# Performance work log

Measured on AMD Instinct MI355X. Metric: run time of the kernel, lower is better.

## Reference

```python
import jax, jax.numpy as jnp
import numpy as np

B, S, D = 2, 2048, 2048
H, KVH = 16, 4
HD = D // H  # 128


def _rope_angles(seq, head_dim):
    theta = 1.0 / (10000.0 ** (jnp.arange(0, head_dim, 2, dtype=jnp.float32) / head_dim))
    ang = jnp.arange(seq, dtype=jnp.float32)[:, None] * theta[None, :]  # [S, HD/2]
    return jnp.cos(ang), jnp.sin(ang)


def _apply_rotary(t, cos, sin):
    # t: [B, S, h, HD]; pairs are (even, odd) along last dim (view_as_complex semantics)
    tr = t[..., 0::2]
    ti = t[..., 1::2]
    c = cos[None, :, None, :]
    s = sin[None, :, None, :]
    out_r = tr * c - ti * s
    out_i = tr * s + ti * c
    return jnp.stack([out_r, out_i], axis=-1).reshape(t.shape)


def setup_inputs() -> dict:
    key = jax.random.key(0)
    ks = jax.random.split(key, 8)
    sd = 1.0 / np.sqrt(D)
    return {
        'x': jax.random.normal(ks[0], (B, S, D), dtype=jnp.float32),
        'wq': jax.random.normal(ks[1], (D, D), dtype=jnp.float32) * sd,
        'bq': jax.random.normal(ks[2], (D,), dtype=jnp.float32) * 0.01,
        'wk': jax.random.normal(ks[3], (D, KVH * HD), dtype=jnp.float32) * sd,
        'bk': jax.random.normal(ks[4], (KVH * HD,), dtype=jnp.float32) * 0.01,
        'wv': jax.random.normal(ks[5], (D, KVH * HD), dtype=jnp.float32) * sd,
        'bv': jax.random.normal(ks[6], (KVH * HD,), dtype=jnp.float32) * 0.01,
        'wo': jax.random.normal(ks[7], (D, D), dtype=jnp.float32) * sd,
    }


def reference(x, wq, bq, wk, bk, wv, bv, wo):
    b, s, d = x.shape
    q = (x @ wq + bq).reshape(b, s, H, HD)
    k = (x @ wk + bk).reshape(b, s, KVH, HD)
    v = (x @ wv + bv).reshape(b, s, KVH, HD)

    cos, sin = _rope_angles(s, HD)
    q = _apply_rotary(q, cos, sin)
    k = _apply_rotary(k, cos, sin)

    repeat = H // KVH
    k = jnp.repeat(k, repeat, axis=2)  # [B, S, H, HD]
    v = jnp.repeat(v, repeat, axis=2)

    scale = 1.0 / np.sqrt(HD)
    att_score = jnp.einsum('bqhd,bkhd->bqhk', q, k) * scale  # [B, S, H, S]
    att_weight = jax.nn.softmax(att_score, axis=-1)
    out = jnp.einsum('bqhk,bkhd->bqhd', att_weight, v)
    out = out.reshape(b, s, H * HD)
    return out @ wo
```

## Files before the change

kernel.cpp:

```cpp
#include <hip/hip_runtime.h>
#include <hip/hip_bf16.h>
#include <cstdint>

typedef __attribute__((ext_vector_type(4))) float f32x4;
typedef __attribute__((ext_vector_type(16))) float f32x16;
typedef __attribute__((ext_vector_type(8))) short bf16x8;
typedef __attribute__((ext_vector_type(4))) unsigned int u32x4;
typedef unsigned short u16;
typedef unsigned int u32;

__device__ __forceinline__ u16 f2b(float x) {
  __hip_bfloat16 h = __float2bfloat16(x);
  return *reinterpret_cast<u16*>(&h);
}

__device__ __forceinline__ u32 pk(float a, float b) {
  return ((u32)f2b(b) << 16) | (u32)f2b(a);
}

__device__ __forceinline__ void gload16(const void* g, void* l) {
  __builtin_amdgcn_global_load_lds((const __attribute__((address_space(1))) u32*)g,
                                   (__attribute__((address_space(3))) u32*)l, 16, 0, 0);
}


__global__ void cvt_f32_bf16(const float* __restrict__ in, u16* __restrict__ out, int n4) {
  int idx = (blockIdx.x * 256 + threadIdx.x);
  if (idx < n4) {
    const float4 v = *(const float4*)(in + (size_t)idx * 4);
    u16* o = out + (size_t)idx * 4;
    o[0] = f2b(v.x); o[1] = f2b(v.y); o[2] = f2b(v.z); o[3] = f2b(v.w);
  }
}

__global__ void w_transpose_cvt(const float* __restrict__ w0, const float* __restrict__ w1,
                                const float* __restrict__ w2, int b0, int b1,
                                int N0, int N1, int N2,
                                u16* __restrict__ out, int K) {
  __shared__ float tile[32][33];
  int k0 = blockIdx.x * 32, n0 = blockIdx.y * 32;
  const float* src; int srcN; int c0;
  if (n0 < b0)      { src = w0; srcN = N0; c0 = n0; }
  else if (n0 < b1) { src = w1; srcN = N1; c0 = n0 - b0; }
  else              { src = w2; srcN = N2; c0 = n0 - b1; }
  int tx = threadIdx.x & 31, ty = threadIdx.x >> 5;
#pragma unroll
  for (int j = 0; j < 32; j += 8)
    tile[ty + j][tx] = src[(size_t)(k0 + ty + j) * srcN + c0 + tx];
  __syncthreads();
#pragma unroll
  for (int j = 0; j < 32; j += 8)
    out[(size_t)(n0 + ty + j) * K + k0 + tx] = f2b(tile[tx][ty + j]);
}

__global__ void pack_bias(const float* __restrict__ bq, const float* __restrict__ bk,
                          const float* __restrict__ bv, float* __restrict__ out) {
  int i = blockIdx.x * 256 + threadIdx.x;
  if (i < 3072) out[i] = (i < 2048) ? bq[i] : ((i < 2560) ? bk[i - 2048] : bv[i - 2560]);
}

__global__ void v_transpose_cvt(const float* __restrict__ qkv, u16* __restrict__ vt) {
  __shared__ float tile[32][33];
  int s0 = blockIdx.x * 32;
  int d0 = blockIdx.y * 32;
  int z = blockIdx.z;
  int b = z >> 2, kvh = z & 3;
  int tx = threadIdx.x & 31, ty = threadIdx.x >> 5;
#pragma unroll
  for (int j = 0; j < 32; j += 8)
    tile[ty + j][tx] = qkv[((size_t)(b * 2048 + s0 + ty + j)) * 3072 + 2560 + kvh * 128 + d0 + tx];
  __syncthreads();
#pragma unroll
  for (int j = 0; j < 32; j += 8)
    vt[((size_t)z * 128 + d0 + ty + j) * 2048 + s0 + tx] = f2b(tile[tx][ty + j]);
}

__global__ void rope_cvt(const float* __restrict__ qkv, u16* __restrict__ out,
                         int lognh, int col0, float scale) {
  int idx = blockIdx.x * 256 + threadIdx.x;
  int i = idx & 63;
  int nh = 1 << lognh;
  int h = (idx >> 6) & (nh - 1);
  int bs = idx >> (6 + lognh);
  int s = bs & 2047;
  int b = bs >> 11;
  const float* src = qkv + (size_t)bs * 3072 + col0 + h * 128 + 2 * i;
  float tr = src[0], ti = src[1];
  float theta = expf(-(float)i * 0.14391156831212787f);
  float ang = (float)s * theta;
  float sv, cv;
  sincosf(ang, &sv, &cv);
  float orr = (tr * cv - ti * sv) * scale;
  float oii = (tr * sv + ti * cv) * scale;
  u16* dst = out + (((size_t)(b * nh + h) * 2048 + s) * 128 + 2 * i);
  dst[0] = f2b(orr);
  dst[1] = f2b(oii);
}

__global__ __launch_bounds__(256) void gemm_bt_bf16(
    const u16* __restrict__ A, const u16* __restrict__ Bt,
    const float* __restrict__ bias, float* __restrict__ C,
    int M, int N, int K) {
  __shared__ u16 As[128 * 32];
  __shared__ u16 Bs[128 * 32];
  const int tid = threadIdx.x;
  const int lane = tid & 63;
  const int w = tid >> 6;
  const int wr = w >> 1, wc = w & 1;
  const int m0 = blockIdx.y * 128;
  const int n0 = blockIdx.x * 128;

  f32x4 acc[4][4] = {};

  for (int k0 = 0; k0 < K; k0 += 32) {
#pragma unroll
    for (int it = 0; it < 2; ++it) {
      int c = tid + it * 256;
      int row = c >> 2;
      int off = (c & 3) * 8;
      gload16(A + (size_t)(m0 + row) * K + k0 + off, (u16*)As + w * 512 + it * 2048);
      gload16(Bt + (size_t)(n0 + row) * K + k0 + off, (u16*)Bs + w * 512 + it * 2048);
    }
    __syncthreads();
    const int col8 = (lane >> 4) * 8;
    bf16x8 a[4], bfr[4];
#pragma unroll
    for (int m = 0; m < 4; ++m)
      a[m] = *(const bf16x8*)&As[(wr * 64 + m * 16 + (lane & 15)) * 32 + col8];
#pragma unroll
    for (int n = 0; n < 4; ++n)
      bfr[n] = *(const bf16x8*)&Bs[(wc * 64 + n * 16 + (lane & 15)) * 32 + col8];
#pragma unroll
    for (int m = 0; m < 4; ++m)
#pragma unroll
      for (int n = 0; n < 4; ++n)
        acc[m][n] = __builtin_amdgcn_mfma_f32_16x16x32_bf16(a[m], bfr[n], acc[m][n], 0, 0, 0);
    __syncthreads();
  }

#pragma unroll
  for (int m = 0; m < 4; ++m) {
    int row = m0 + wr * 64 + m * 16 + ((lane >> 4) << 2);
#pragma unroll
    for (int n = 0; n < 4; ++n) {
      int col = n0 + wc * 64 + n * 16 + (lane & 15);
      float bvv = bias ? bias[col] : 0.f;
      float* cp = C + (size_t)row * N + col;
#pragma unroll
      for (int r = 0; r < 4; ++r) cp[(size_t)r * N] = acc[m][n][r] + bvv;
    }
  }
}

__global__ __launch_bounds__(256) void flash_attn(
    const u16* __restrict__ Qr, const u16* __restrict__ Kr,
    const u16* __restrict__ Vt, u16* __restrict__ Att) {
  __shared__ u16 Ks[2][64 * 128];
  __shared__ u16 Vs[2][128 * 64];
  const int tid = threadIdx.x, lane = tid & 63, w = tid >> 6;
  const int lo = lane & 31, hi = lane >> 5;
  const int q0 = blockIdx.x * 128 + w * 32;
  const int h = blockIdx.y, b = blockIdx.z;
  const int kvh = h >> 2;

  const char* Khead = (const char*)(Kr + (size_t)(b * 4 + kvh) * 2048 * 128);
  const char* Vhead = (const char*)(Vt + (size_t)(b * 4 + kvh) * 128 * 2048);

  bf16x8 qf[8];
  {
    const u16* qp = Qr + ((size_t)(b * 16 + h) * 2048 + q0 + lo) * 128 + hi * 8;
#pragma unroll
    for (int ds = 0; ds < 8; ++ds) qf[ds] = *(const bf16x8*)(qp + ds * 16);
  }

  int koff[4], voff[4];
#pragma unroll
  for (int it = 0; it < 4; ++it) {
    int c = tid + it * 256;
    int krow = c >> 4;
    koff[it] = krow * 256 + (((c & 15) * 16) ^ ((krow & 7) << 4));
    int vrow = c >> 3;
    voff[it] = vrow * 4096 + (((c & 7) * 16) ^ ((vrow & 7) << 4));
  }

#define STAGE(bufi, t)                                                \
  {                                                                   \
    _Pragma("unroll")                                                 \
    for (int it = 0; it < 4; ++it) {                                  \
      gload16(Khead + (size_t)(t) * 16384 + koff[it],                 \
              (u16*)Ks[bufi] + it * 2048 + w * 512);                  \
      gload16(Vhead + (size_t)(t) * 128 + voff[it],                   \
              (u16*)Vs[bufi] + it * 2048 + w * 512);                  \
    }                                                                 \
  }

  f32x16 o0 = {}, o1 = {}, o2 = {}, o3 = {};
  float m_run = -3.0e38f, l_run = 0.f;
  const int swz = (lane & 7) << 4;
  const int hi16 = hi * 16;

  STAGE(0, 0);
  __syncthreads();

  int buf = 0;
  for (int t = 0; t < 32; ++t) {
    if (t < 31) { STAGE(buf ^ 1, t + 1); }

    const char* Kb = (const char*)Ks[buf];
    const char* Vb = (const char*)Vs[buf];

    f32x16 sc0 = {}, sc1 = {};
    __builtin_amdgcn_s_setprio(1);
#pragma unroll
    for (int ds = 0; ds < 8; ++ds) {
      bf16x8 kf = *(const bf16x8*)(Kb + lo * 256 + ((ds * 32 + hi16) ^ swz));
      sc0 = __builtin_amdgcn_mfma_f32_32x32x16_bf16(kf, qf[ds], sc0, 0, 0, 0);
    }
#pragma unroll
    for (int ds = 0; ds < 8; ++ds) {
      bf16x8 kf = *(const bf16x8*)(Kb + (32 + lo) * 256 + ((ds * 32 + hi16) ^ swz));
      sc1 = __builtin_amdgcn_mfma_f32_32x32x16_bf16(kf, qf[ds], sc1, 0, 0, 0);
    }
    __builtin_amdgcn_s_setprio(0);

    float pmax = sc0[0];
#pragma unroll
    for (int r = 1; r < 16; ++r) pmax = fmaxf(pmax, sc0[r]);
#pragma unroll
    for (int r = 0; r < 16; ++r) pmax = fmaxf(pmax, sc1[r]);
    pmax = fmaxf(pmax, __shfl_xor(pmax, 32, 64));

    if (!__all(pmax - m_run <= 8.0f)) {
      float mnew = fmaxf(m_run, pmax);
      float rs = __expf(m_run - mnew);
      m_run = mnew;
      l_run *= rs;
#pragma unroll
      for (int r = 0; r < 16; ++r) {
        float rsr = __shfl(rs, (r & 3) + 8 * (r >> 2) + 4 * hi, 64);
        o0[r] *= rsr; o1[r] *= rsr; o2[r] *= rsr; o3[r] *= rsr;
      }
    }

    float lsum = 0.f;
#pragma unroll
    for (int r = 0; r < 16; ++r) { float p = __expf(sc0[r] - m_run); sc0[r] = p; lsum += p; }
#pragma unroll
    for (int r = 0; r < 16; ++r) { float p = __expf(sc1[r] - m_run); sc1[r] = p; lsum += p; }
    lsum += __shfl_xor(lsum, 32, 64);
    l_run += lsum;

#define MKPA(P, s, dst)                                               \
    {                                                                 \
      u32 a0 = pk(P[8*(s)+0], P[8*(s)+1]);                            \
      u32 a1 = pk(P[8*(s)+2], P[8*(s)+3]);                            \
      u32 b0 = pk(P[8*(s)+4], P[8*(s)+5]);                            \
      u32 b1 = pk(P[8*(s)+6], P[8*(s)+7]);                            \
      u32 t0 = hi ? a0 : b0, t1 = hi ? a1 : b1;                       \
      u32 r0 = __shfl_xor(t0, 32, 64), r1 = __shfl_xor(t1, 32, 64);   \
      u32x4 wv;                                                       \
      wv[0] = hi ? r0 : a0; wv[1] = hi ? r1 : a1;                     \
      wv[2] = hi ? b0 : r0; wv[3] = hi ? b1 : r1;                     \
      dst = __builtin_bit_cast(bf16x8, wv);                           \
    }
    bf16x8 pa0, pa1, pa2, pa3;
    MKPA(sc0, 0, pa0)
    MKPA(sc0, 1, pa1)
    MKPA(sc1, 0, pa2)
    MKPA(sc1, 1, pa3)

    __builtin_amdgcn_s_setprio(1);
#define PVN(on, n)                                                                                    \
    {                                                                                                 \
      const char* vrb = Vb + ((n) * 32 + lo) * 128;                                                   \
      on = __builtin_amdgcn_mfma_f32_32x32x16_bf16(pa0, *(const bf16x8*)(vrb + ((0   + hi16) ^ swz)), on, 0, 0, 0); \
      on = __builtin_amdgcn_mfma_f32_32x32x16_bf16(pa1, *(const bf16x8*)(vrb + ((32  + hi16) ^ swz)), on, 0, 0, 0); \
      on = __builtin_amdgcn_mfma_f32_32x32x16_bf16(pa2, *(const bf16x8*)(vrb + ((64  + hi16) ^ swz)), on, 0, 0, 0); \
      on = __builtin_amdgcn_mfma_f32_32x32x16_bf16(pa3, *(const bf16x8*)(vrb + ((96  + hi16) ^ swz)), on, 0, 0, 0); \
    }
    PVN(o0, 0)
    PVN(o1, 1)
    PVN(o2, 2)
    PVN(o3, 3)
    __builtin_amdgcn_s_setprio(0);

    __syncthreads();
    buf ^= 1;
  }

  float inv = 1.0f / l_run;
  size_t rowbase = (size_t)(b * 2048 + q0);
#pragma unroll
  for (int r = 0; r < 16; ++r) {
    int rr = (r & 3) + 8 * (r >> 2) + 4 * hi;
    float invr = __shfl(inv, rr, 64);
    u16* op = Att + (rowbase + rr) * 2048 + h * 128 + lo;
    op[0]  = f2b(o0[r] * invr);
    op[32] = f2b(o1[r] * invr);
    op[64] = f2b(o2[r] * invr);
    op[96] = f2b(o3[r] * invr);
  }
}


extern "C" void kernel_launch(void* const* d_in, const int* in_sizes, int n_in,
                              void* d_out, int out_size, void* d_ws, size_t ws_size,
                              hipStream_t stream) {
  const float* x  = (const float*)d_in[0];
  const float* wq = (const float*)d_in[1];
  const float* bq = (const float*)d_in[2];
  const float* wk = (const float*)d_in[3];
  const float* bk = (const float*)d_in[4];
  const float* wv = (const float*)d_in[5];
  const float* bv = (const float*)d_in[6];
  const float* wo = (const float*)d_in[7];
  float* out = (float*)d_out;
  char* ws = (char*)d_ws;

  u16*   x_bf   = (u16*)  (ws + 0);
  u16*   att    = (u16*)  (ws + 0);
  u16*   wqkv_t = (u16*)  (ws + 16777216);
  u16*   wo_t   = (u16*)  (ws + 29360128);
  float* biasq  = (float*)(ws + 37748736);
  float* qkv    = (float*)(ws + 37761024);
  u16*   q_r    = (u16*)  (ws + 88092672);
  u16*   k_r    = (u16*)  (ws + 104869888);
  u16*   v_t    = (u16*)  (ws + 109064192);

  cvt_f32_bf16<<<8192, 256, 0, stream>>>(x, x_bf, 2097152);
  w_transpose_cvt<<<dim3(64, 96), 256, 0, stream>>>(wq, wk, wv, 2048, 2560,
                                                    2048, 512, 512, wqkv_t, 2048);
  w_transpose_cvt<<<dim3(64, 64), 256, 0, stream>>>(wo, wo, wo, 2048, 2560,
                                                    2048, 2048, 2048, wo_t, 2048);
  pack_bias<<<12, 256, 0, stream>>>(bq, bk, bv, biasq);

  gemm_bt_bf16<<<dim3(24, 32), 256, 0, stream>>>(x_bf, wqkv_t, biasq, qkv, 4096, 3072, 2048);

  rope_cvt<<<16384, 256, 0, stream>>>(qkv, q_r, 4, 0, 0.08838834764831845f);
  rope_cvt<<<4096, 256, 0, stream>>>(qkv, k_r, 2, 2048, 1.0f);
  v_transpose_cvt<<<dim3(64, 4, 8), 256, 0, stream>>>(qkv, v_t);

  flash_attn<<<dim3(16, 16, 2), 256, 0, stream>>>(q_r, k_r, v_t, att);

  gemm_bt_bf16<<<dim3(16, 32), 256, 0, stream>>>(att, wo_t, nullptr, out, 4096, 2048, 2048);
}
```

Measured before the change: 310.4 us.

## Shrink flash-attention tiles to 64 queries and 32 keys per block

Rewrites the flash attention kernel to use 128-thread blocks covering 64 queries, stepping through keys in 32-wide tiles (64 iterations) instead of 64-wide tiles. The grid grows to twice as many blocks and LDS per block drops by half, aiming for more resident blocks per CU and better latency hiding. K/V staging now computes offsets inline, and V uses a new swizzle suited to the 64-byte rows. The cost is more loop iterations, more barriers and more softmax rescale checks per key, plus a redundant final stage load.

Measured after the change: 294.6 us. -5.1%, faster.

```diff
diff --git a/kernel.cpp b/kernel.cpp
--- a/kernel.cpp
+++ b/kernel.cpp
@@ -21,6 +21,13 @@
 __device__ __forceinline__ void gload16(const void* g, void* l) {
   __builtin_amdgcn_global_load_lds((const __attribute__((address_space(1))) u32*)g,
                                    (__attribute__((address_space(3))) u32*)l, 16, 0, 0);
+}
+
+__device__ __forceinline__ float xmax32(float x) {
+  return fmaxf(x, __shfl_xor(x, 32, 64));
+}
+__device__ __forceinline__ float xsum32(float x) {
+  return x + __shfl_xor(x, 32, 64);
 }
 
 
@@ -152,14 +159,14 @@
   }
 }
 
-__global__ __launch_bounds__(256) void flash_attn(
+__global__ __launch_bounds__(128, 3) void flash_attn(
     const u16* __restrict__ Qr, const u16* __restrict__ Kr,
     const u16* __restrict__ Vt, u16* __restrict__ Att) {
-  __shared__ u16 Ks[2][64 * 128];
-  __shared__ u16 Vs[2][128 * 64];
+  __shared__ u16 Ks[2][32 * 128];
+  __shared__ u16 Vs[2][128 * 32];
   const int tid = threadIdx.x, lane = tid & 63, w = tid >> 6;
   const int lo = lane & 31, hi = lane >> 5;
-  const int q0 = blockIdx.x * 128 + w * 32;
+  const int q0 = blockIdx.x * 64 + w * 32;
   const int h = blockIdx.y, b = blockIdx.z;
   const int kvh = h >> 2;
 
@@ -173,62 +180,53 @@
     for (int ds = 0; ds < 8; ++ds) qf[ds] = *(const bf16x8*)(qp + ds * 16);
   }
 
-  int koff[4], voff[4];
-#pragma unroll
-  for (int it = 0; it < 4; ++it) {
-    int c = tid + it * 256;
-    int krow = c >> 4;
-    koff[it] = krow * 256 + (((c & 15) * 16) ^ ((krow & 7) << 4));
-    int vrow = c >> 3;
-    voff[it] = vrow * 4096 + (((c & 7) * 16) ^ ((vrow & 7) << 4));
-  }
-
-#define STAGE(bufi, t)                                                \
-  {                                                                   \
-    _Pragma("unroll")                                                 \
-    for (int it = 0; it < 4; ++it) {                                  \
-      gload16(Khead + (size_t)(t) * 16384 + koff[it],                 \
-              (u16*)Ks[bufi] + it * 2048 + w * 512);                  \
-      gload16(Vhead + (size_t)(t) * 128 + voff[it],                   \
-              (u16*)Vs[bufi] + it * 2048 + w * 512);                  \
-    }                                                                 \
+#define STAGE(bufi, t)                                                        \
+  {                                                                           \
+    _Pragma("unroll")                                                         \
+    for (int it = 0; it < 4; ++it) {                                          \
+      int c = it * 128 + tid;                                                 \
+      int krow = c >> 4;                                                      \
+      int koff = krow * 256 + ((c & 15) << 4 ^ ((krow & 7) << 4));            \
+      gload16(Khead + (size_t)(t) * 8192 + koff,                              \
+              (u16*)Ks[bufi] + it * 1024 + w * 512);                          \
+      int vrow = c >> 2;                                                      \
+      int voff = vrow * 4096 + ((c & 3) << 4 ^ (((vrow >> 1) & 3) << 4));     \
+      gload16(Vhead + (size_t)(t) * 64 + voff,                                \
+              (u16*)Vs[bufi] + it * 1024 + w * 512);                          \
+    }                                                                         \
   }
 
   f32x16 o0 = {}, o1 = {}, o2 = {}, o3 = {};
   float m_run = -3.0e38f, l_run = 0.f;
-  const int swz = (lane & 7) << 4;
+  const int swz = (lo & 7) << 4;
+  const int vswz = ((lo >> 1) & 3) << 4;
   const int hi16 = hi * 16;
 
   STAGE(0, 0);
   __syncthreads();
 
   int buf = 0;
-  for (int t = 0; t < 32; ++t) {
-    if (t < 31) { STAGE(buf ^ 1, t + 1); }
+  for (int t = 0; t < 64; ++t) {
+    int tn = (t < 63) ? t + 1 : 63;
+    STAGE(buf ^ 1, tn);
 
     const char* Kb = (const char*)Ks[buf];
     const char* Vb = (const char*)Vs[buf];
 
-    f32x16 sc0 = {}, sc1 = {};
+    f32x16 sc = {};
     __builtin_amdgcn_s_setprio(1);
 #pragma unroll
     for (int ds = 0; ds < 8; ++ds) {
       bf16x8 kf = *(const bf16x8*)(Kb + lo * 256 + ((ds * 32 + hi16) ^ swz));
-      sc0 = __builtin_amdgcn_mfma_f32_32x32x16_bf16(kf, qf[ds], sc0, 0, 0, 0);
-    }
-#pragma unroll
-    for (int ds = 0; ds < 8; ++ds) {
-      bf16x8 kf = *(const bf16x8*)(Kb + (32 + lo) * 256 + ((ds * 32 + hi16) ^ swz));
-      sc1 = __builtin_amdgcn_mfma_f32_32x32x16_bf16(kf, qf[ds], sc1, 0, 0, 0);
+      sc = __builtin_amdgcn_mfma_f32_32x32x16_bf16(kf, qf[ds], sc, 0, 0, 0);
     }
     __builtin_amdgcn_s_setprio(0);
 
-    float pmax = sc0[0];
-#pragma unroll
-    for (int r = 1; r < 16; ++r) pmax = fmaxf(pmax, sc0[r]);
-#pragma unroll
-    for (int r = 0; r < 16; ++r) pmax = fmaxf(pmax, sc1[r]);
-    pmax = fmaxf(pmax, __shfl_xor(pmax, 32, 64));
+    float m01 = fmaxf(fmaxf(sc[0], sc[1]), fmaxf(sc[2], sc[3]));
+    float m23 = fmaxf(fmaxf(sc[4], sc[5]), fmaxf(sc[6], sc[7]));
+    float m45 = fmaxf(fmaxf(sc[8], sc[9]), fmaxf(sc[10], sc[11]));
+    float m67 = fmaxf(fmaxf(sc[12], sc[13]), fmaxf(sc[14], sc[15]));
+    float pmax = xmax32(fmaxf(fmaxf(m01, m23), fmaxf(m45, m67)));
 
     if (!__all(pmax - m_run <= 8.0f)) {
       float mnew = fmaxf(m_run, pmax);
@@ -244,39 +242,35 @@
 
     float lsum = 0.f;
 #pragma unroll
-    for (int r = 0; r < 16; ++r) { float p = __expf(sc0[r] - m_run); sc0[r] = p; lsum += p; }
-#pragma unroll
-    for (int r = 0; r < 16; ++r) { float p = __expf(sc1[r] - m_run); sc1[r] = p; lsum += p; }
-    lsum += __shfl_xor(lsum, 32, 64);
-    l_run += lsum;
-
-#define MKPA(P, s, dst)                                               \
-    {                                                                 \
-      u32 a0 = pk(P[8*(s)+0], P[8*(s)+1]);                            \
-      u32 a1 = pk(P[8*(s)+2], P[8*(s)+3]);                            \
-      u32 b0 = pk(P[8*(s)+4], P[8*(s)+5]);                            \
-      u32 b1 = pk(P[8*(s)+6], P[8*(s)+7]);                            \
-      u32 t0 = hi ? a0 : b0, t1 = hi ? a1 : b1;                       \
-      u32 r0 = __shfl_xor(t0, 32, 64), r1 = __shfl_xor(t1, 32, 64);   \
-      u32x4 wv;                                                       \
-      wv[0] = hi ? r0 : a0; wv[1] = hi ? r1 : a1;                     \
-      wv[2] = hi ? b0 : r0; wv[3] = hi ? b1 : r1;                     \
-      dst = __builtin_bit_cast(bf16x8, wv);                           \
-    }
-    bf16x8 pa0, pa1, pa2, pa3;
-    MKPA(sc0, 0, pa0)
-    MKPA(sc0, 1, pa1)
-    MKPA(sc1, 0, pa2)
-    MKPA(sc1, 1, pa3)
+    for (int r = 0; r < 16; ++r) { float p = __expf(sc[r] - m_run); sc[r] = p; lsum += p; }
+    l_run += xsum32(lsum);
+
+    bf16x8 pa0, pa1;
+    {
+      u32 a0 = pk(sc[0], sc[1]),   a1 = pk(sc[2], sc[3]);
+      u32 b0 = pk(sc[4], sc[5]),   b1 = pk(sc[6], sc[7]);
+      u32 t0 = hi ? a0 : b0, t1 = hi ? a1 : b1;
+      u32 r0 = __shfl_xor(t0, 32, 64), r1 = __shfl_xor(t1, 32, 64);
+      u32x4 w0;
+      w0[0] = hi ? r0 : a0; w0[1] = hi ? r1 : a1;
+      w0[2] = hi ? b0 : r0; w0[3] = hi ? b1 : r1;
+      pa0 = __builtin_bit_cast(bf16x8, w0);
+      u32 c0 = pk(sc[8], sc[9]),   c1 = pk(sc[10], sc[11]);
+      u32 d0 = pk(sc[12], sc[13]), d1 = pk(sc[14], sc[15]);
+      u32 t2 = hi ? c0 : d0, t3 = hi ? c1 : d1;
+      u32 r2 = __shfl_xor(t2, 32, 64), r3 = __shfl_xor(t3, 32, 64);
+      u32x4 w1;
+      w1[0] = hi ? r2 : c0; w1[1] = hi ? r3 : c1;
+      w1[2] = hi ? d0 : r2; w1[3] = hi ? d1 : r3;
+      pa1 = __builtin_bit_cast(bf16x8, w1);
+    }
 
     __builtin_amdgcn_s_setprio(1);
-#define PVN(on, n)                                                                                    \
-    {                                                                                                 \
-      const char* vrb = Vb + ((n) * 32 + lo) * 128;                                                   \
-      on = __builtin_amdgcn_mfma_f32_32x32x16_bf16(pa0, *(const bf16x8*)(vrb + ((0   + hi16) ^ swz)), on, 0, 0, 0); \
-      on = __builtin_amdgcn_mfma_f32_32x32x16_bf16(pa1, *(const bf16x8*)(vrb + ((32  + hi16) ^ swz)), on, 0, 0, 0); \
-      on = __builtin_amdgcn_mfma_f32_32x32x16_bf16(pa2, *(const bf16x8*)(vrb + ((64  + hi16) ^ swz)), on, 0, 0, 0); \
-      on = __builtin_amdgcn_mfma_f32_32x32x16_bf16(pa3, *(const bf16x8*)(vrb + ((96  + hi16) ^ swz)), on, 0, 0, 0); \
+#define PVN(on, n)                                                                                     \
+    {                                                                                                  \
+      const char* vrb = Vb + ((n) * 32 + lo) * 64;                                                     \
+      on = __builtin_amdgcn_mfma_f32_32x32x16_bf16(pa0, *(const bf16x8*)(vrb + ((0  + hi16) ^ vswz)), on, 0, 0, 0); \
+      on = __builtin_amdgcn_mfma_f32_32x32x16_bf16(pa1, *(const bf16x8*)(vrb + ((32 + hi16) ^ vswz)), on, 0, 0, 0); \
     }
     PVN(o0, 0)
     PVN(o1, 1)
@@ -340,7 +334,7 @@
   rope_cvt<<<4096, 256, 0, stream>>>(qkv, k_r, 2, 2048, 1.0f);
   v_transpose_cvt<<<dim3(64, 4, 8), 256, 0, stream>>>(qkv, v_t);
 
-  flash_attn<<<dim3(16, 16, 2), 256, 0, stream>>>(q_r, k_r, v_t, att);
+  flash_attn<<<dim3(32, 16, 2), 128, 0, stream>>>(q_r, k_r, v_t, att);
 
   gemm_bt_bf16<<<dim3(16, 32), 256, 0, stream>>>(att, wo_t, nullptr, out, 4096, 2048, 2048);
 }
```
